# Kernel optimization log

Measured on AMD Instinct MI355X. Metric: run time of the kernel, lower is better.

## Reference

```python
import jax, jax.numpy as jnp
import numpy as np

N_NODES = 50000
N_EDGES = 800000
IN_DIM = 128
HID2 = 128   # 2 * hid_dim
HID = 64     # hid_dim
PROJ = 64    # proj_dim


def _glorot(key, shape):
    fan_in, fan_out = shape
    lim = (6.0 / (fan_in + fan_out)) ** 0.5
    return jax.random.uniform(key, shape, jnp.float32, -lim, lim)


def setup_inputs() -> dict:
    key = jax.random.key(0)
    ks = jax.random.split(key, 9)
    x = jax.random.normal(ks[0], (N_NODES, IN_DIM), jnp.float32)
    edge_index = jax.random.randint(ks[1], (2, N_EDGES), 0, N_NODES, dtype=jnp.int32)
    return {
        "x": x,
        "edge_index": edge_index,
        "W1": _glorot(ks[2], (IN_DIM, HID2)),
        "b1": jnp.zeros((HID2,), jnp.float32),
        "W2": _glorot(ks[3], (HID2, HID2)),
        "b2": jnp.zeros((HID2,), jnp.float32),
        "W3": _glorot(ks[4], (HID2, HID)),
        "b3": jnp.zeros((HID,), jnp.float32),
        "Wp": _glorot(ks[5], (HID, PROJ)),  # projection Linear has bias=False (dropout=0 passed as bias arg)
    }


def _gcn_conv(x, W, b, src, dst, d_inv_sqrt, n):
    # PyG GCNConv: h = x W; out[dst] += norm(src,dst) * h[src]; out += b
    h = x @ W
    coef = d_inv_sqrt[src] * d_inv_sqrt[dst]          # [E+N]
    agg = jax.ops.segment_sum(h[src] * coef[:, None], dst, num_segments=n)
    return agg + b


def reference(x, edge_index, W1, b1, W2, b2, W3, b3, Wp):
    n = x.shape[0]
    loops = jnp.arange(n, dtype=edge_index.dtype)
    src = jnp.concatenate([edge_index[0], loops])
    dst = jnp.concatenate([edge_index[1], loops])
    deg = jax.ops.segment_sum(jnp.ones_like(src, jnp.float32), dst, num_segments=n)
    d_inv_sqrt = jnp.where(deg > 0, jax.lax.rsqrt(deg), 0.0)

    # encoder.embed: stacked GCNConv + ReLU (no dropout in embed)
    h = jax.nn.relu(_gcn_conv(x, W1, b1, src, dst, d_inv_sqrt, n))
    h = jax.nn.relu(_gcn_conv(h, W2, b2, src, dst, d_inv_sqrt, n))
    h = jax.nn.relu(_gcn_conv(h, W3, b3, src, dst, d_inv_sqrt, n))

    # projection head (Linear, no bias) + ReLU
    p = jax.nn.relu(h @ Wp)

    # F.normalize(p, dim=1), eps=1e-12
    norm = jnp.linalg.norm(p, axis=1, keepdims=True)
    return p / jnp.maximum(norm, 1e-12)
```

## Files before the change

kernel.cpp:

```cpp
#include <hip/hip_runtime.h>
#include <hip/hip_fp16.h>

typedef _Float16 half8v __attribute__((ext_vector_type(8)));
typedef _Float16 half4v __attribute__((ext_vector_type(4)));
typedef _Float16 half2v __attribute__((ext_vector_type(2)));
typedef float f32x4 __attribute__((ext_vector_type(4)));


__global__ void cvt_wz(const float* __restrict__ W1, const float* __restrict__ W2,
                       const float* __restrict__ W3,
                       _Float16* __restrict__ Wt1, _Float16* __restrict__ Wt2,
                       _Float16* __restrict__ Wt3,
                       int* __restrict__ cnt, int n) {
    int i = blockIdx.x * blockDim.x + threadIdx.x;
    if (i < 16384) {
        int nn = i >> 7, kk = i & 127;
        Wt1[i] = (_Float16)W1[kk * 128 + nn];
    } else if (i < 32768) {
        int j = i - 16384; int nn = j >> 7, kk = j & 127;
        Wt2[j] = (_Float16)W2[kk * 128 + nn];
    } else if (i < 40960) {
        int j = i - 32768; int nn = j >> 7, kk = j & 127;
        Wt3[j] = (_Float16)W3[kk * 64 + nn];
    }
    int z = i - 40960;
    if (z >= 0 && z < n) cnt[z] = 0;
}


__global__ void count_rank(const int* __restrict__ dst, int E, int* __restrict__ cnt,
                           unsigned short* __restrict__ rank) {
    int e = blockIdx.x * blockDim.x + threadIdx.x;
    if (e < E) rank[e] = (unsigned short)atomicAdd(&cnt[dst[e]], 1);
}

__global__ __launch_bounds__(256) void scanA(const int* __restrict__ cnt,
                                             int* __restrict__ row_ptr,
                                             int* __restrict__ blockSums,
                                             float* __restrict__ dis, int n) {
    __shared__ int s[256];
    int t = threadIdx.x;
    int base = blockIdx.x * 1024 + t * 4;
    int v0 = (base + 0 < n) ? cnt[base + 0] : 0;
    int v1 = (base + 1 < n) ? cnt[base + 1] : 0;
    int v2 = (base + 2 < n) ? cnt[base + 2] : 0;
    int v3 = (base + 3 < n) ? cnt[base + 3] : 0;
    if (base + 0 < n) dis[base + 0] = rsqrtf((float)(v0 + 1));
    if (base + 1 < n) dis[base + 1] = rsqrtf((float)(v1 + 1));
    if (base + 2 < n) dis[base + 2] = rsqrtf((float)(v2 + 1));
    if (base + 3 < n) dis[base + 3] = rsqrtf((float)(v3 + 1));
    int tsum = v0 + v1 + v2 + v3;
    s[t] = tsum;
    __syncthreads();
    for (int off = 1; off < 256; off <<= 1) {
        int u = (t >= off) ? s[t - off] : 0;
        __syncthreads();
        s[t] += u;
        __syncthreads();
    }
    int excl = s[t] - tsum;
    if (base + 0 < n) row_ptr[base + 0] = excl;
    if (base + 1 < n) row_ptr[base + 1] = excl + v0;
    if (base + 2 < n) row_ptr[base + 2] = excl + v0 + v1;
    if (base + 3 < n) row_ptr[base + 3] = excl + v0 + v1 + v2;
    if (t == 255) blockSums[blockIdx.x] = s[255];
}

__global__ __launch_bounds__(256) void scanC(int* __restrict__ row_ptr,
                                             const int* __restrict__ blockSums,
                                             int n, int E, int B) {
    __shared__ int soff;
    int t = threadIdx.x;
    if (t < 64) {
        int v = (t < B) ? blockSums[t] : 0;
        int orig = v;
        for (int off = 1; off < 64; off <<= 1) {
            int u = __shfl_up(v, off, 64);
            if (t >= off) v += u;
        }
        if (t == (int)blockIdx.x) soff = v - orig;
    }
    __syncthreads();
    int off = soff;
    int base = blockIdx.x * 1024 + t * 4;
    #pragma unroll
    for (int j = 0; j < 4; ++j)
        if (base + j < n) row_ptr[base + j] += off;
    if (blockIdx.x == 0 && t == 0) row_ptr[n] = E;
}

__global__ void fill_nr(const int* __restrict__ src, const int* __restrict__ dst,
                        const unsigned short* __restrict__ rank, int E,
                        const int* __restrict__ row_ptr, const float* __restrict__ dis,
                        unsigned int* __restrict__ edges) {
    int e = blockIdx.x * blockDim.x + threadIdx.x;
    if (e >= E) return;
    int d = dst[e], s = src[e];
    int slot = row_ptr[d] + (int)rank[e];
    float coef = dis[s] * dis[d];
    edges[slot] = (unsigned)s |
                  ((unsigned)__half_as_ushort(__float2half_rn(coef)) << 16);
}

__device__ __forceinline__ void unpack_edge(unsigned int w, int& s, float& c) {
    s = (int)(w & 0xffffu);
    c = __half2float(__ushort_as_half((unsigned short)(w >> 16)));
}


template <int N, bool F32IN>
__global__ __launch_bounds__(256) void gemm_mfma(const void* __restrict__ Xin,
                                                 const _Float16* __restrict__ Wt,
                                                 _Float16* __restrict__ Y, int M) {
    constexpr int NT = N / 16;
    int wave = threadIdx.x >> 6;
    int lane = threadIdx.x & 63;
    int m0 = blockIdx.x * 64 + wave * 16;
    int r = lane & 15;
    int kb = lane >> 4;
    int ar = m0 + r; if (ar >= M) ar = M - 1;
    f32x4 acc[NT] = {};
    #pragma unroll
    for (int kk = 0; kk < 128; kk += 32) {
        half8v a;
        if constexpr (F32IN) {
            const float* arow = (const float*)Xin + (size_t)ar * 128 + kb * 8 + kk;
            float4 f0 = *(const float4*)arow;
            float4 f1 = *(const float4*)(arow + 4);
            a = (half8v){(_Float16)f0.x, (_Float16)f0.y, (_Float16)f0.z, (_Float16)f0.w,
                         (_Float16)f1.x, (_Float16)f1.y, (_Float16)f1.z, (_Float16)f1.w};
        } else {
            a = *(const half8v*)((const _Float16*)Xin + (size_t)ar * 128 + kb * 8 + kk);
        }
        #pragma unroll
        for (int c = 0; c < NT; ++c) {
            half8v b = *(const half8v*)(Wt + (size_t)(c * 16 + r) * 128 + kk + kb * 8);
            acc[c] = __builtin_amdgcn_mfma_f32_16x16x32_f16(a, b, acc[c], 0, 0, 0);
        }
    }
    #pragma unroll
    for (int j = 0; j < 4; ++j) {
        int row = m0 + kb * 4 + j;
        if (row < M) {
            #pragma unroll
            for (int c = 0; c < NT; ++c)
                Y[(size_t)row * N + c * 16 + r] = (_Float16)acc[c][j];
        }
    }
}


template <int NOUT>
__global__ __launch_bounds__(1024) void agg_gemm(const __half2* __restrict__ hp,
                                                 const int* __restrict__ row_ptr,
                                                 const unsigned int* __restrict__ edges,
                                                 const float* __restrict__ dis,
                                                 const float* __restrict__ bias,
                                                 const _Float16* __restrict__ Wt,
                                                 _Float16* __restrict__ Y, int n) {
    __shared__ _Float16 As[16][136];
    int t = threadIdx.x;
    int wave = t >> 6;
    int lane = t & 63;
    int m0 = blockIdx.x * 16;
    int node = m0 + wave;
    float ox = 0.f, oy = 0.f;
    if (node < n) {
        int beg = row_ptr[node], end = row_ptr[node + 1];
        float di = dis[node];
        float cs = di * di;
        float2 sv = __half22float2(hp[(size_t)node * 64 + lane]);
        float2 a0 = {cs * sv.x, cs * sv.y};
        float2 a1 = {0.f, 0.f}, a2 = {0.f, 0.f}, a3 = {0.f, 0.f};
        int e = beg;
        for (; e + 4 <= end; e += 4) {
            unsigned int w0 = edges[e], w1 = edges[e + 1], w2 = edges[e + 2], w3 = edges[e + 3];
            int s0, s1, s2, s3; float c0, c1, c2, c3;
            unpack_edge(w0, s0, c0); unpack_edge(w1, s1, c1);
            unpack_edge(w2, s2, c2); unpack_edge(w3, s3, c3);
            float2 u0 = __half22float2(hp[(size_t)s0 * 64 + lane]);
            float2 u1 = __half22float2(hp[(size_t)s1 * 64 + lane]);
            float2 u2 = __half22float2(hp[(size_t)s2 * 64 + lane]);
            float2 u3 = __half22float2(hp[(size_t)s3 * 64 + lane]);
            a0.x += c0 * u0.x; a0.y += c0 * u0.y;
            a1.x += c1 * u1.x; a1.y += c1 * u1.y;
            a2.x += c2 * u2.x; a2.y += c2 * u2.y;
            a3.x += c3 * u3.x; a3.y += c3 * u3.y;
        }
        for (; e < end; ++e) {
            int s0; float c0;
            unpack_edge(edges[e], s0, c0);
            float2 u0 = __half22float2(hp[(size_t)s0 * 64 + lane]);
            a0.x += c0 * u0.x; a0.y += c0 * u0.y;
        }
        float2 bv = ((const float2*)bias)[lane];
        ox = fmaxf(a0.x + a1.x + a2.x + a3.x + bv.x, 0.f);
        oy = fmaxf(a0.y + a1.y + a2.y + a3.y + bv.y, 0.f);
    }
    *(half2v*)&As[wave][2 * lane] = (half2v){(_Float16)ox, (_Float16)oy};
    __syncthreads();
    constexpr int CT = NOUT / 16;
    if (wave < CT) {
        int r = lane & 15;
        int kb = lane >> 4;
        f32x4 acc = {};
        #pragma unroll
        for (int kk = 0; kk < 128; kk += 32) {
            half8v a = *(const half8v*)&As[r][kb * 8 + kk];
            half8v b = *(const half8v*)(Wt + (size_t)(wave * 16 + r) * 128 + kk + kb * 8);
            acc = __builtin_amdgcn_mfma_f32_16x16x32_f16(a, b, acc, 0, 0, 0);
        }
        #pragma unroll
        for (int j = 0; j < 4; ++j) {
            int row = m0 + kb * 4 + j;
            if (row < n)
                Y[(size_t)row * NOUT + wave * 16 + r] = (_Float16)acc[j];
        }
    }
}


__global__ __launch_bounds__(256) void agg_proj(const _Float16* __restrict__ h,
                                                const int* __restrict__ row_ptr,
                                                const unsigned int* __restrict__ edges,
                                                const float* __restrict__ dis,
                                                const float* __restrict__ b3,
                                                const float* __restrict__ Wp,
                                                float* __restrict__ P, int n) {
    __shared__ float oT[64 * 68];
    __shared__ float Ws[64 * 64];
    int t = threadIdx.x;
    int base = blockIdx.x * 64;
    for (int j = t * 4; j < 4096; j += 1024)
        *(float4*)&Ws[j] = *(const float4*)&Wp[j];
    int cg = t & 15;
    int ng = t >> 4;
    int c0 = cg * 4;
    float4 bv = *(const float4*)&b3[c0];
    #pragma unroll
    for (int pass = 0; pass < 4; ++pass) {
        int ni = pass * 16 + ng;
        int node = base + ni;
        float ax = 0.f, ay = 0.f, az = 0.f, aw = 0.f;
        if (node < n) {
            int beg = row_ptr[node], end = row_ptr[node + 1];
            float di = dis[node];
            float cs = di * di;
            half4v sv = *(const half4v*)&h[(size_t)node * 64 + c0];
            ax = cs * (float)sv[0]; ay = cs * (float)sv[1];
            az = cs * (float)sv[2]; aw = cs * (float)sv[3];
            float bx = 0.f, by = 0.f, bz = 0.f, bw = 0.f;
            int e = beg;
            for (; e + 2 <= end; e += 2) {
                unsigned int w0 = edges[e], w1 = edges[e + 1];
                int s0, s1; float cc0, cc1;
                unpack_edge(w0, s0, cc0); unpack_edge(w1, s1, cc1);
                half4v u0 = *(const half4v*)&h[(size_t)s0 * 64 + c0];
                half4v u1 = *(const half4v*)&h[(size_t)s1 * 64 + c0];
                ax += cc0 * (float)u0[0]; ay += cc0 * (float)u0[1];
                az += cc0 * (float)u0[2]; aw += cc0 * (float)u0[3];
                bx += cc1 * (float)u1[0]; by += cc1 * (float)u1[1];
                bz += cc1 * (float)u1[2]; bw += cc1 * (float)u1[3];
            }
            if (e < end) {
                int s0; float cc0;
                unpack_edge(edges[e], s0, cc0);
                half4v u0 = *(const half4v*)&h[(size_t)s0 * 64 + c0];
                ax += cc0 * (float)u0[0]; ay += cc0 * (float)u0[1];
                az += cc0 * (float)u0[2]; aw += cc0 * (float)u0[3];
            }
            ax = fmaxf(ax + bx + bv.x, 0.f);
            ay = fmaxf(ay + by + bv.y, 0.f);
            az = fmaxf(az + bz + bv.z, 0.f);
            aw = fmaxf(aw + bw + bv.w, 0.f);
        }
        oT[(c0 + 0) * 68 + ni] = ax;
        oT[(c0 + 1) * 68 + ni] = ay;
        oT[(c0 + 2) * 68 + ni] = az;
        oT[(c0 + 3) * 68 + ni] = aw;
    }
    __syncthreads();
    float acc[4][4] = {};
    const float* otp = &oT[ng * 4];
    const float* wsp = &Ws[cg * 4];
    #pragma unroll 2
    for (int k = 0; k < 64; ++k) {
        float4 ov = *(const float4*)&otp[k * 68];
        float4 wv = *(const float4*)&wsp[k * 64];
        #pragma unroll
        for (int i = 0; i < 4; ++i) {
            float o = (&ov.x)[i];
            acc[i][0] += o * wv.x;
            acc[i][1] += o * wv.y;
            acc[i][2] += o * wv.z;
            acc[i][3] += o * wv.w;
        }
    }
    #pragma unroll
    for (int i = 0; i < 4; ++i) {
        float4 p;
        p.x = fmaxf(acc[i][0], 0.f);
        p.y = fmaxf(acc[i][1], 0.f);
        p.z = fmaxf(acc[i][2], 0.f);
        p.w = fmaxf(acc[i][3], 0.f);
        float ss = p.x * p.x + p.y * p.y + p.z * p.z + p.w * p.w;
        #pragma unroll
        for (int off = 1; off < 16; off <<= 1) ss += __shfl_xor(ss, off, 64);
        float norm = sqrtf(ss);
        float sc = 1.0f / fmaxf(norm, 1e-12f);
        int node = base + ng * 4 + i;
        if (node < n) {
            p.x *= sc; p.y *= sc; p.z *= sc; p.w *= sc;
            *(float4*)&P[(size_t)node * 64 + cg * 4] = p;
        }
    }
}


static inline size_t ws_align(size_t x) { return (x + 255) & ~(size_t)255; }

extern "C" void kernel_launch(void* const* d_in, const int* in_sizes, int n_in,
                              void* d_out, int out_size, void* d_ws, size_t ws_size,
                              hipStream_t stream) {
    const float* x  = (const float*)d_in[0];
    const int*   ei = (const int*)d_in[1];
    const float* W1 = (const float*)d_in[2];
    const float* b1 = (const float*)d_in[3];
    const float* W2 = (const float*)d_in[4];
    const float* b2 = (const float*)d_in[5];
    const float* W3 = (const float*)d_in[6];
    const float* b3 = (const float*)d_in[7];
    const float* Wp = (const float*)d_in[8];

    int n = in_sizes[0] / 128;
    int E = in_sizes[1] / 2;
    const int* src = ei;
    const int* dst = ei + E;

    char* ws = (char*)d_ws;
    size_t off = 0;
    auto alloc = [&](size_t bytes) -> void* {
        void* p = ws + off;
        off = ws_align(off + bytes);
        return p;
    };
    _Float16* bufA = (_Float16*)alloc((size_t)n * 128 * 2);
    _Float16* bufB = (_Float16*)alloc((size_t)n * 128 * 2);
    _Float16* Wt1  = (_Float16*)alloc(128 * 128 * 2);
    _Float16* Wt2  = (_Float16*)alloc(128 * 128 * 2);
    _Float16* Wt3  = (_Float16*)alloc(64 * 128 * 2);
    int*   cnt      = (int*)alloc((size_t)n * 4);
    float* dis      = (float*)alloc((size_t)n * 4);
    int*   row_ptr  = (int*)alloc((size_t)(n + 1) * 4);
    unsigned short* rank = (unsigned short*)alloc((size_t)E * 2);
    unsigned int* edges = (unsigned int*)alloc((size_t)E * 4);
    int*   blockSums = (int*)alloc(256);
    (void)off; (void)ws_size;

    int B = (n + 1023) / 1024;
    int wz = 40960 + n;
    cvt_wz<<<(wz + 255) / 256, 256, 0, stream>>>(W1, W2, W3, Wt1, Wt2, Wt3, cnt, n);
    count_rank<<<(E + 255) / 256, 256, 0, stream>>>(dst, E, cnt, rank);
    scanA<<<B, 256, 0, stream>>>(cnt, row_ptr, blockSums, dis, n);
    scanC<<<B, 256, 0, stream>>>(row_ptr, blockSums, n, E, B);
    fill_nr<<<(E + 255) / 256, 256, 0, stream>>>(src, dst, rank, E, row_ptr, dis, edges);

    int gblocks = (n + 63) / 64;
    int fblocks = (n + 15) / 16;
    int pblocks = (n + 63) / 64;
    float* outp = (float*)d_out;

    gemm_mfma<128, true><<<gblocks, 256, 0, stream>>>(x, Wt1, bufA, n);
    agg_gemm<128><<<fblocks, 1024, 0, stream>>>((const __half2*)bufA, row_ptr, edges, dis, b1,
                                                Wt2, bufB, n);
    agg_gemm<64><<<fblocks, 1024, 0, stream>>>((const __half2*)bufB, row_ptr, edges, dis, b2,
                                               Wt3, bufA, n);
    agg_proj<<<pblocks, 256, 0, stream>>>(bufA, row_ptr, edges, dis, b3, Wp, outp, n);
}
```

Measured before the change: 233.4 us.

## Process nodes in degree-sorted order to balance aggregation work per block

Builds a counting-sort permutation of nodes by in-degree (histogram in scanA, prefix scan, atomic scatter) and has the aggregation kernels process nodes in that order, writing results back to the original node index. The goal is for the 16 waves of a block to have similar edge counts, which reduces tail imbalance within a block. In exchange it adds two small kernels plus histogram atomics, and it loses locality: neighbouring rows in a block are no longer contiguous, so output writes scatter and dst-ordered locality is gone.

```diff
diff --git a/kernel.cpp b/kernel.cpp
--- a/kernel.cpp
+++ b/kernel.cpp
@@ -6,12 +6,14 @@
 typedef _Float16 half2v __attribute__((ext_vector_type(2)));
 typedef float f32x4 __attribute__((ext_vector_type(4)));
 
+#define NBIN 1024
+
 
 __global__ void cvt_wz(const float* __restrict__ W1, const float* __restrict__ W2,
                        const float* __restrict__ W3,
                        _Float16* __restrict__ Wt1, _Float16* __restrict__ Wt2,
                        _Float16* __restrict__ Wt3,
-                       int* __restrict__ cnt, int n) {
+                       int* __restrict__ cnt, int* __restrict__ hist, int n) {
     int i = blockIdx.x * blockDim.x + threadIdx.x;
     if (i < 16384) {
         int nn = i >> 7, kk = i & 127;
@@ -23,6 +25,7 @@
         int j = i - 32768; int nn = j >> 7, kk = j & 127;
         Wt3[j] = (_Float16)W3[kk * 64 + nn];
     }
+    if (i < NBIN) hist[i] = 0;
     int z = i - 40960;
     if (z >= 0 && z < n) cnt[z] = 0;
 }
@@ -37,7 +40,8 @@
 __global__ __launch_bounds__(256) void scanA(const int* __restrict__ cnt,
                                              int* __restrict__ row_ptr,
                                              int* __restrict__ blockSums,
-                                             float* __restrict__ dis, int n) {
+                                             float* __restrict__ dis,
+                                             int* __restrict__ hist, int n) {
     __shared__ int s[256];
     int t = threadIdx.x;
     int base = blockIdx.x * 1024 + t * 4;
@@ -45,10 +49,10 @@
     int v1 = (base + 1 < n) ? cnt[base + 1] : 0;
     int v2 = (base + 2 < n) ? cnt[base + 2] : 0;
     int v3 = (base + 3 < n) ? cnt[base + 3] : 0;
-    if (base + 0 < n) dis[base + 0] = rsqrtf((float)(v0 + 1));
-    if (base + 1 < n) dis[base + 1] = rsqrtf((float)(v1 + 1));
-    if (base + 2 < n) dis[base + 2] = rsqrtf((float)(v2 + 1));
-    if (base + 3 < n) dis[base + 3] = rsqrtf((float)(v3 + 1));
+    if (base + 0 < n) { dis[base + 0] = rsqrtf((float)(v0 + 1)); atomicAdd(&hist[min(v0, NBIN - 1)], 1); }
+    if (base + 1 < n) { dis[base + 1] = rsqrtf((float)(v1 + 1)); atomicAdd(&hist[min(v1, NBIN - 1)], 1); }
+    if (base + 2 < n) { dis[base + 2] = rsqrtf((float)(v2 + 1)); atomicAdd(&hist[min(v2, NBIN - 1)], 1); }
+    if (base + 3 < n) { dis[base + 3] = rsqrtf((float)(v3 + 1)); atomicAdd(&hist[min(v3, NBIN - 1)], 1); }
     int tsum = v0 + v1 + v2 + v3;
     s[t] = tsum;
     __syncthreads();
@@ -87,6 +91,35 @@
     for (int j = 0; j < 4; ++j)
         if (base + j < n) row_ptr[base + j] += off;
     if (blockIdx.x == 0 && t == 0) row_ptr[n] = E;
+}
+
+__global__ __launch_bounds__(256) void scan_hist(int* __restrict__ hist) {
+    __shared__ int s[256];
+    int t = threadIdx.x;
+    int v0 = hist[t * 4], v1 = hist[t * 4 + 1], v2 = hist[t * 4 + 2], v3 = hist[t * 4 + 3];
+    int tsum = v0 + v1 + v2 + v3;
+    s[t] = tsum;
+    __syncthreads();
+    for (int off = 1; off < 256; off <<= 1) {
+        int u = (t >= off) ? s[t - off] : 0;
+        __syncthreads();
+        s[t] += u;
+        __syncthreads();
+    }
+    int excl = s[t] - tsum;
+    hist[t * 4 + 0] = excl;
+    hist[t * 4 + 1] = excl + v0;
+    hist[t * 4 + 2] = excl + v0 + v1;
+    hist[t * 4 + 3] = excl + v0 + v1 + v2;
+}
+
+__global__ void scatter_order(const int* __restrict__ cnt, int* __restrict__ histoff,
+                              int* __restrict__ order, int n) {
+    int i = blockIdx.x * blockDim.x + threadIdx.x;
+    if (i >= n) return;
+    int bin = min(cnt[i], NBIN - 1);
+    int pos = atomicAdd(&histoff[bin], 1);
+    order[pos] = i;
 }
 
 __global__ void fill_nr(const int* __restrict__ src, const int* __restrict__ dst,
@@ -157,15 +190,18 @@
                                                  const float* __restrict__ dis,
                                                  const float* __restrict__ bias,
                                                  const _Float16* __restrict__ Wt,
+                                                 const int* __restrict__ order,
                                                  _Float16* __restrict__ Y, int n) {
     __shared__ _Float16 As[16][136];
+    __shared__ int nid[16];
     int t = threadIdx.x;
     int wave = t >> 6;
     int lane = t & 63;
     int m0 = blockIdx.x * 16;
-    int node = m0 + wave;
+    int node = (m0 + wave < n) ? order[m0 + wave] : -1;
+    if (lane == 0) nid[wave] = node;
     float ox = 0.f, oy = 0.f;
-    if (node < n) {
+    if (node >= 0) {
         int beg = row_ptr[node], end = row_ptr[node + 1];
         float di = dis[node];
         float cs = di * di;
@@ -212,8 +248,8 @@
         }
         #pragma unroll
         for (int j = 0; j < 4; ++j) {
-            int row = m0 + kb * 4 + j;
-            if (row < n)
+            int row = nid[kb * 4 + j];
+            if (row >= 0)
                 Y[(size_t)row * NOUT + wave * 16 + r] = (_Float16)acc[j];
         }
     }
@@ -226,6 +262,7 @@
                                                 const float* __restrict__ dis,
                                                 const float* __restrict__ b3,
                                                 const float* __restrict__ Wp,
+                                                const int* __restrict__ order,
                                                 float* __restrict__ P, int n) {
     __shared__ float oT[64 * 68];
     __shared__ float Ws[64 * 64];
@@ -240,9 +277,9 @@
     #pragma unroll
     for (int pass = 0; pass < 4; ++pass) {
         int ni = pass * 16 + ng;
-        int node = base + ni;
+        int node = (base + ni < n) ? order[base + ni] : -1;
         float ax = 0.f, ay = 0.f, az = 0.f, aw = 0.f;
-        if (node < n) {
+        if (node >= 0) {
             int beg = row_ptr[node], end = row_ptr[node + 1];
             float di = dis[node];
             float cs = di * di;
@@ -308,8 +345,9 @@
         for (int off = 1; off < 16; off <<= 1) ss += __shfl_xor(ss, off, 64);
         float norm = sqrtf(ss);
         float sc = 1.0f / fmaxf(norm, 1e-12f);
-        int node = base + ng * 4 + i;
-        if (node < n) {
+        int oi = base + ng * 4 + i;
+        if (oi < n) {
+            int node = order[oi];
             p.x *= sc; p.y *= sc; p.z *= sc; p.w *= sc;
             *(float4*)&P[(size_t)node * 64 + cg * 4] = p;
         }
@@ -354,15 +392,19 @@
     int*   row_ptr  = (int*)alloc((size_t)(n + 1) * 4);
     unsigned short* rank = (unsigned short*)alloc((size_t)E * 2);
     unsigned int* edges = (unsigned int*)alloc((size_t)E * 4);
+    int*   order    = (int*)alloc((size_t)n * 4);
+    int*   hist     = (int*)alloc(NBIN * 4);
     int*   blockSums = (int*)alloc(256);
     (void)off; (void)ws_size;
 
     int B = (n + 1023) / 1024;
     int wz = 40960 + n;
-    cvt_wz<<<(wz + 255) / 256, 256, 0, stream>>>(W1, W2, W3, Wt1, Wt2, Wt3, cnt, n);
+    cvt_wz<<<(wz + 255) / 256, 256, 0, stream>>>(W1, W2, W3, Wt1, Wt2, Wt3, cnt, hist, n);
     count_rank<<<(E + 255) / 256, 256, 0, stream>>>(dst, E, cnt, rank);
-    scanA<<<B, 256, 0, stream>>>(cnt, row_ptr, blockSums, dis, n);
+    scanA<<<B, 256, 0, stream>>>(cnt, row_ptr, blockSums, dis, hist, n);
     scanC<<<B, 256, 0, stream>>>(row_ptr, blockSums, n, E, B);
+    scan_hist<<<1, 256, 0, stream>>>(hist);
+    scatter_order<<<(n + 255) / 256, 256, 0, stream>>>(cnt, hist, order, n);
     fill_nr<<<(E + 255) / 256, 256, 0, stream>>>(src, dst, rank, E, row_ptr, dis, edges);
 
     int gblocks = (n + 63) / 64;
@@ -372,8 +414,8 @@
 
     gemm_mfma<128, true><<<gblocks, 256, 0, stream>>>(x, Wt1, bufA, n);
     agg_gemm<128><<<fblocks, 1024, 0, stream>>>((const __half2*)bufA, row_ptr, edges, dis, b1,
-                                                Wt2, bufB, n);
+                                                Wt2, order, bufB, n);
     agg_gemm<64><<<fblocks, 1024, 0, stream>>>((const __half2*)bufB, row_ptr, edges, dis, b2,
-                                               Wt3, bufA, n);
-    agg_proj<<<pblocks, 256, 0, stream>>>(bufA, row_ptr, edges, dis, b3, Wp, outp, n);
-}
+                                               Wt3, order, bufA, n);
+    agg_proj<<<pblocks, 256, 0, stream>>>(bufA, row_ptr, edges, dis, b3, Wp, order, outp, n);
+}
```

Measured after the change: 503.5 us. +115.8%, slower.
